# Optimization experiments

Hardware: AMD Instinct MI355X
Metric: run time of the kernel (lower is better)

## Reference

```python
import jax, jax.numpy as jnp
import numpy as np

H = 16          # num_attention_heads
HD = 64         # attention_head_size
ALPHA = 1.5
BANDWIDTH = 1.0
A_EXP = 0.5     # sinkhorn-like exponent 'a'
DIST_SCALE = float(HD)  # alpha < 2 => scale by head_size
EPS = 1e-12     # F.normalize eps


def setup_inputs() -> dict:
    key = jax.random.key(0)
    ks = jax.random.split(key, 5)
    B, L, D = 2, 1024, 1024
    w_scale = 0.02  # keep distances in a non-degenerate range for the power-law kernel
    x = jax.random.normal(ks[0], (B, L, D), dtype=jnp.float32)
    WQ = jax.random.normal(ks[1], (D, D), dtype=jnp.float32) * w_scale
    WK = jax.random.normal(ks[2], (D, D), dtype=jnp.float32) * w_scale
    WV = jax.random.normal(ks[3], (D, D), dtype=jnp.float32) * w_scale
    WO = jax.random.normal(ks[4], (D, D), dtype=jnp.float32) * w_scale
    z = jnp.zeros((D,), dtype=jnp.float32)
    return {"x": x, "WQ": WQ, "bQ": z, "WK": WK, "bK": z,
            "WV": WV, "bV": z, "WO": WO, "bO": z}


def _heads(t, B, L):
    # [B, L, H*HD] -> [B, H, L, HD]
    return t.reshape(B, L, H, HD).transpose(0, 2, 1, 3)


def reference(x, WQ, bQ, WK, bK, WV, bV, WO, bO):
    B, L, D = x.shape
    q = _heads(x @ WQ + bQ, B, L)   # [B,H,L,HD]
    k = _heads(x @ WK + bK, B, L)
    v = _heads(x @ WV + bV, B, L)

    # torch.cdist(q, k, p=2): pairwise euclidean distance [B,H,L,L]
    q2 = jnp.sum(q * q, axis=-1)                      # [B,H,L]
    k2 = jnp.sum(k * k, axis=-1)                      # [B,H,L]
    qk = jnp.einsum('bhid,bhjd->bhij', q, k)          # [B,H,L,L]
    d2 = q2[..., :, None] + k2[..., None, :] - 2.0 * qk
    g_dist = jnp.sqrt(jnp.maximum(d2, EPS)) / DIST_SCALE

    # alpha < 2: power-law kernel (1 + g/sqrt(bw))^(-(d_intrinsic + alpha))
    attn_score = (1.0 + g_dist / np.sqrt(BANDWIDTH)) ** (-(HD + ALPHA))

    # a > 0: Sinkhorn-style row/col renormalization
    N_R = jnp.sum(attn_score, axis=-1)                # [B,H,L] row sums
    N_C = jnp.sum(attn_score, axis=-2)                # [B,H,L] col sums
    K_tilde = (N_R ** (-A_EXP))[..., :, None] * attn_score * (N_C ** (-A_EXP))[..., None, :]

    # F.normalize(p=1, dim=3); entries are positive so |.| sum == sum
    attention_probs = K_tilde / jnp.maximum(jnp.sum(K_tilde, axis=-1, keepdims=True), EPS)

    out = jnp.einsum('bhij,bhjd->bhid', attention_probs, v)   # [B,H,L,HD]
    out = out.transpose(0, 2, 1, 3).reshape(B, L, H * HD)
    return out @ WO + bO
```

## Files before the change

### kernel.cpp

```cpp
#include <hip/hip_runtime.h>
#include <math.h>


typedef __attribute__((ext_vector_type(8))) short short8;
typedef __attribute__((ext_vector_type(4))) float f32x4;

__device__ inline unsigned short f2bf(float f) {
  unsigned int u = __float_as_uint(f);
  unsigned int r = (u + 0x7FFFu + ((u >> 16) & 1u)) >> 16;
  return (unsigned short)r;
}
__device__ inline float bf2f(unsigned short s) {
  return __uint_as_float(((unsigned int)s) << 16);
}
__device__ inline float score_fn(float dot, float sq) {
  float d2 = fmaxf(fmaf(-2.f, dot, sq), 1e-12f);
  float sd = __builtin_amdgcn_sqrtf(d2);
  float lg = __builtin_amdgcn_logf(fmaf(sd, 0.015625f, 1.0f));
  return __builtin_amdgcn_exp2f(-65.5f * lg);
}
__device__ inline unsigned int cvtpk(float lo, float hi) {
  unsigned int r;
  asm("v_cvt_pk_bf16_f32 %0, %1, %2" : "=v"(r) : "v"(lo), "v"(hi));
  return r;
}
#define GLD16(lptr, gptr)                                                      \
  __builtin_amdgcn_global_load_lds(                                            \
      (const __attribute__((address_space(1))) void*)(gptr),                   \
      (__attribute__((address_space(3))) void*)(lptr), 16, 0, 0)

__global__ __launch_bounds__(256) void cvt_f32_bf16(const float* __restrict__ in,
                                                    unsigned short* __restrict__ out) {
  int i = blockIdx.x * 256 + threadIdx.x;
  float4 v = ((const float4*)in)[i];
  out[4 * i + 0] = f2bf(v.x);
  out[4 * i + 1] = f2bf(v.y);
  out[4 * i + 2] = f2bf(v.z);
  out[4 * i + 3] = f2bf(v.w);
}

__global__ __launch_bounds__(256) void wtrans4(const float* __restrict__ W0,
                                               const float* __restrict__ W1,
                                               const float* __restrict__ W2,
                                               const float* __restrict__ W3,
                                               unsigned short* __restrict__ T0,
                                               unsigned short* __restrict__ T1,
                                               unsigned short* __restrict__ T2,
                                               unsigned short* __restrict__ T3) {
  int z = blockIdx.z;
  const float* W = z == 0 ? W0 : z == 1 ? W1 : z == 2 ? W2 : W3;
  unsigned short* WT = z == 0 ? T0 : z == 1 ? T1 : z == 2 ? T2 : T3;
  __shared__ float T[32][33];
  int k0 = blockIdx.x * 32, n0 = blockIdx.y * 32;
  int c = threadIdx.x & 31, r8 = threadIdx.x >> 5;
#pragma unroll
  for (int it = 0; it < 4; ++it) {
    int rr = r8 + it * 8;
    T[rr][c] = W[(size_t)(k0 + rr) * 1024 + n0 + c];
  }
  __syncthreads();
#pragma unroll
  for (int it = 0; it < 4; ++it) {
    int rr = r8 + it * 8;
    WT[(size_t)(n0 + rr) * 1024 + k0 + c] = f2bf(T[c][rr]);
  }
}

__global__ __launch_bounds__(256) void gemm_st(const unsigned short* __restrict__ A,
                                               const unsigned short* __restrict__ B0,
                                               const unsigned short* __restrict__ B1,
                                               const unsigned short* __restrict__ B2,
                                               const float* __restrict__ c0,
                                               const float* __restrict__ c1,
                                               const float* __restrict__ c2,
                                               void* __restrict__ Y0,
                                               void* __restrict__ Y1,
                                               void* __restrict__ Y2,
                                               int m0, int m1, int m2) {
  int z = blockIdx.z;
  const unsigned short* BT = z == 0 ? B0 : z == 1 ? B1 : B2;
  const float* bias = z == 0 ? c0 : z == 1 ? c1 : c2;
  void* Y = z == 0 ? Y0 : z == 1 ? Y1 : Y2;
  int mode = z == 0 ? m0 : z == 1 ? m1 : m2;

  __shared__ __align__(16) unsigned short As[2][64 * 64];
  __shared__ __align__(16) unsigned short Bs[2][64 * 64];
  int tid = threadIdx.x;
  int w = tid >> 6, l = tid & 63, g = l >> 4, l15 = l & 15;
  int bm = blockIdx.x * 64, bn = blockIdx.y * 64;
  const int arow = w * 16 + l15;
  const int x7 = l15 & 7;

  const int i0s = tid, i1s = 256 + tid;
  const int r0 = i0s >> 3, s0 = (i0s & 7) ^ (r0 & 7);
  const int r1 = i1s >> 3, s1 = (i1s & 7) ^ (r1 & 7);

  GLD16(&As[0][i0s * 8], &A[(size_t)(bm + r0) * 1024 + s0 * 8]);
  GLD16(&As[0][i1s * 8], &A[(size_t)(bm + r1) * 1024 + s1 * 8]);
  GLD16(&Bs[0][i0s * 8], &BT[(size_t)(bn + r0) * 1024 + s0 * 8]);
  GLD16(&Bs[0][i1s * 8], &BT[(size_t)(bn + r1) * 1024 + s1 * 8]);

  f32x4 acc[4];
#pragma unroll
  for (int t = 0; t < 4; ++t)
#pragma unroll
    for (int r = 0; r < 4; ++r) acc[t][r] = 0.f;

  __syncthreads();
  for (int t = 0; t < 16; ++t) {
    int cur = t & 1;
    if (t < 15) {
      int kn = (t + 1) * 64;
      GLD16(&As[cur ^ 1][i0s * 8], &A[(size_t)(bm + r0) * 1024 + kn + s0 * 8]);
      GLD16(&As[cur ^ 1][i1s * 8], &A[(size_t)(bm + r1) * 1024 + kn + s1 * 8]);
      GLD16(&Bs[cur ^ 1][i0s * 8], &BT[(size_t)(bn + r0) * 1024 + kn + s0 * 8]);
      GLD16(&Bs[cur ^ 1][i1s * 8], &BT[(size_t)(bn + r1) * 1024 + kn + s1 * 8]);
    }
#pragma unroll
    for (int kc = 0; kc < 2; ++kc) {
      short8 a = *(const short8*)&As[cur][arow * 64 + ((kc * 4 + g) ^ x7) * 8];
#pragma unroll
      for (int tt = 0; tt < 4; ++tt) {
        short8 b = *(const short8*)&Bs[cur][(tt * 16 + l15) * 64 + ((kc * 4 + g) ^ x7) * 8];
        acc[tt] = __builtin_amdgcn_mfma_f32_16x16x32_bf16(a, b, acc[tt], 0, 0, 0);
      }
    }
    __syncthreads();
  }

#pragma unroll
  for (int t = 0; t < 4; ++t) {
    int n = bn + 16 * t + l15;
    float bv = bias[n];
#pragma unroll
    for (int r = 0; r < 4; ++r) {
      int m = bm + w * 16 + 4 * g + r;
      float v = acc[t][r] + bv;
      if (mode == 0) {
        int b = m >> 10, ll = m & 1023, h = n >> 6, hd = n & 63;
        ((unsigned short*)Y)[(((size_t)(b * 16 + h) * 1024) + ll) * 64 + hd] = f2bf(v);
      } else if (mode == 1) {
        int b = m >> 10, ll = m & 1023, h = n >> 6, hd = n & 63;
        int jp = (ll & ~31) | (((ll >> 2) & 3) * 8 + ((ll >> 4) & 1) * 4 + (ll & 3));
        ((unsigned short*)Y)[(((size_t)(b * 16 + h) * 64) + hd) * 1024 + jp] = f2bf(v);
      } else {
        ((float*)Y)[(size_t)m * 1024 + n] = v;
      }
    }
  }
}

__global__ __launch_bounds__(256) void sqnorm(const unsigned short* __restrict__ Qb,
                                              const unsigned short* __restrict__ Kb,
                                              float* __restrict__ q2,
                                              float* __restrict__ k2) {
  int row = blockIdx.x * 256 + threadIdx.x;
  const unsigned short* src = blockIdx.y ? Kb : Qb;
  float* dst = blockIdx.y ? k2 : q2;
  const short8* p = (const short8*)&src[(size_t)row * 64];
  float s = 0.f;
#pragma unroll
  for (int c = 0; c < 8; ++c) {
    short8 v = p[c];
#pragma unroll
    for (int e = 0; e < 8; ++e) {
      float f = bf2f((unsigned short)v[e]);
      s = fmaf(f, f, s);
    }
  }
  dst[row] = s;
}

__global__ __launch_bounds__(256) void colsum_mfma(const unsigned short* __restrict__ Qb,
                                                   const unsigned short* __restrict__ Kb,
                                                   const float* __restrict__ q2,
                                                   const float* __restrict__ k2,
                                                   float* __restrict__ rnc) {
  __shared__ __align__(16) unsigned short Qd[2][64 * 64];
  __shared__ __align__(16) float q2s[1024];
  int bh = blockIdx.x, jt = blockIdx.y;
  int tid = threadIdx.x, w = tid >> 6, l = tid & 63;
  int g = l >> 4, l15 = l & 15;
  const int x7 = l15 & 7;
  const unsigned short* Qp = Qb + (size_t)bh * 65536;
  const unsigned short* Kp = Kb + (size_t)bh * 65536;
  int j = jt * 64 + w * 16 + l15;

  const int i0s = tid, i1s = 256 + tid;
  const int r0 = i0s >> 3, s0 = (i0s & 7) ^ (r0 & 7);
  const int r1 = i1s >> 3, s1 = (i1s & 7) ^ (r1 & 7);

  GLD16(&q2s[tid * 4], q2 + (size_t)bh * 1024 + tid * 4);
  GLD16(&Qd[0][i0s * 8], Qp + (size_t)r0 * 64 + s0 * 8);
  GLD16(&Qd[0][i1s * 8], Qp + (size_t)r1 * 64 + s1 * 8);

  short8 bk0 = *(const short8*)&Kp[(size_t)j * 64 + 8 * g];
  short8 bk1 = *(const short8*)&Kp[(size_t)j * 64 + 32 + 8 * g];
  float k2j = k2[(size_t)bh * 1024 + j];
  float colacc = 0.f;

  __syncthreads();
  for (int t = 0; t < 16; ++t) {
    int cur = t & 1;
    if (t < 15) {
      int inx = (t + 1) * 64;
      GLD16(&Qd[cur ^ 1][i0s * 8], Qp + (size_t)(inx + r0) * 64 + s0 * 8);
      GLD16(&Qd[cur ^ 1][i1s * 8], Qp + (size_t)(inx + r1) * 64 + s1 * 8);
    }
    const unsigned short* Ql = Qd[cur];
#pragma unroll
    for (int tp = 0; tp < 4; ++tp) {
      int rowb = (16 * tp + l15) * 64;
      short8 a0 = *(const short8*)&Ql[rowb + ((g) ^ x7) * 8];
      short8 a1 = *(const short8*)&Ql[rowb + ((4 + g) ^ x7) * 8];
      f32x4 cf;
#pragma unroll
      for (int r = 0; r < 4; ++r) cf[r] = 0.f;
      cf = __builtin_amdgcn_mfma_f32_16x16x32_bf16(a0, bk0, cf, 0, 0, 0);
      cf = __builtin_amdgcn_mfma_f32_16x16x32_bf16(a1, bk1, cf, 0, 0, 0);
      float4 qv = *(const float4*)&q2s[t * 64 + 16 * tp + 4 * g];
      colacc += score_fn(cf[0], qv.x + k2j);
      colacc += score_fn(cf[1], qv.y + k2j);
      colacc += score_fn(cf[2], qv.z + k2j);
      colacc += score_fn(cf[3], qv.w + k2j);
    }
    __syncthreads();
  }
  colacc += __shfl_xor(colacc, 16);
  colacc += __shfl_xor(colacc, 32);
  if (l < 16) rnc[(size_t)bh * 1024 + jt * 64 + w * 16 + l] = __builtin_amdgcn_rsqf(colacc);
}

__global__ __launch_bounds__(256) void attn_mfma(const unsigned short* __restrict__ Qb,
                                                 const unsigned short* __restrict__ Kb,
                                                 const unsigned short* __restrict__ VTp,
                                                 const float* __restrict__ q2,
                                                 const float* __restrict__ k2,
                                                 const float* __restrict__ rnc,
                                                 unsigned short* __restrict__ AO) {
  __shared__ __align__(16) unsigned short Kd[2][64 * 64];
  __shared__ __align__(16) unsigned short Vd[2][64 * 64];
  __shared__ __align__(16) float k2s[1024];
  __shared__ __align__(16) float rns[1024];
  int bh = blockIdx.x;
  int tid = threadIdx.x, w = tid >> 6, l = tid & 63;
  int g = l >> 4, l15 = l & 15;
  const int x7 = l15 & 7;
  int it0 = blockIdx.y * 64 + w * 16;
  const unsigned short* Qp = Qb + (size_t)bh * 65536;
  const unsigned short* Kp = Kb + (size_t)bh * 65536;
  const unsigned short* Vp = VTp + (size_t)bh * 65536;
  int b = bh >> 4, h = bh & 15;

  const int i0s = tid, i1s = 256 + tid;
  const int r0 = i0s >> 3, s0 = (i0s & 7) ^ (r0 & 7);
  const int r1 = i1s >> 3, s1 = (i1s & 7) ^ (r1 & 7);

  GLD16(&k2s[tid * 4], k2 + (size_t)bh * 1024 + tid * 4);
  GLD16(&rns[tid * 4], rnc + (size_t)bh * 1024 + tid * 4);
  GLD16(&Kd[0][i0s * 8], Kp + (size_t)r0 * 64 + s0 * 8);
  GLD16(&Kd[0][i1s * 8], Kp + (size_t)r1 * 64 + s1 * 8);
  GLD16(&Vd[0][i0s * 8], Vp + (size_t)r0 * 1024 + s0 * 8);
  GLD16(&Vd[0][i1s * 8], Vp + (size_t)r1 * 1024 + s1 * 8);

  short8 bq0 = *(const short8*)&Qp[(size_t)(it0 + l15) * 64 + 8 * g];
  short8 bq1 = *(const short8*)&Qp[(size_t)(it0 + l15) * 64 + 32 + 8 * g];
  float q2l = q2[(size_t)bh * 1024 + it0 + l15];

  f32x4 o[4];
#pragma unroll
  for (int t = 0; t < 4; ++t)
#pragma unroll
    for (int r = 0; r < 4; ++r) o[t][r] = 0.f;
  float dacc = 0.f;

  __syncthreads();
  for (int t = 0; t < 16; ++t) {
    int cur = t & 1;
    if (t < 15) {
      int j0n = (t + 1) * 64;
      GLD16(&Kd[cur ^ 1][i0s * 8], Kp + (size_t)(j0n + r0) * 64 + s0 * 8);
      GLD16(&Kd[cur ^ 1][i1s * 8], Kp + (size_t)(j0n + r1) * 64 + s1 * 8);
      GLD16(&Vd[cur ^ 1][i0s * 8], Vp + (size_t)r0 * 1024 + j0n + s0 * 8);
      GLD16(&Vd[cur ^ 1][i1s * 8], Vp + (size_t)r1 * 1024 + j0n + s1 * 8);
    }
    const unsigned short* Kl = Kd[cur];
    const unsigned short* Vl = Vd[cur];
    int j0 = t * 64;
    float sc[16];
#pragma unroll
    for (int tp = 0; tp < 4; ++tp) {
      int rowb = (16 * tp + l15) * 64;
      short8 a0 = *(const short8*)&Kl[rowb + ((g) ^ x7) * 8];
      short8 a1 = *(const short8*)&Kl[rowb + ((4 + g) ^ x7) * 8];
      f32x4 cf;
#pragma unroll
      for (int r = 0; r < 4; ++r) cf[r] = 0.f;
      cf = __builtin_amdgcn_mfma_f32_16x16x32_bf16(a0, bq0, cf, 0, 0, 0);
      cf = __builtin_amdgcn_mfma_f32_16x16x32_bf16(a1, bq1, cf, 0, 0, 0);
      float4 kv = *(const float4*)&k2s[j0 + 16 * tp + 4 * g];
      float4 rv = *(const float4*)&rns[j0 + 16 * tp + 4 * g];
      sc[tp * 4 + 0] = score_fn(cf[0], q2l + kv.x) * rv.x;
      sc[tp * 4 + 1] = score_fn(cf[1], q2l + kv.y) * rv.y;
      sc[tp * 4 + 2] = score_fn(cf[2], q2l + kv.z) * rv.z;
      sc[tp * 4 + 3] = score_fn(cf[3], q2l + kv.w) * rv.w;
    }
#pragma unroll
    for (int i = 0; i < 16; ++i) dacc += sc[i];
    int pi0[4], pi1[4];
    pi0[0] = (int)cvtpk(sc[0], sc[1]);
    pi0[1] = (int)cvtpk(sc[2], sc[3]);
    pi0[2] = (int)cvtpk(sc[4], sc[5]);
    pi0[3] = (int)cvtpk(sc[6], sc[7]);
    pi1[0] = (int)cvtpk(sc[8], sc[9]);
    pi1[1] = (int)cvtpk(sc[10], sc[11]);
    pi1[2] = (int)cvtpk(sc[12], sc[13]);
    pi1[3] = (int)cvtpk(sc[14], sc[15]);
    short8 pa0 = *(short8*)pi0;
    short8 pa1 = *(short8*)pi1;
#pragma unroll
    for (int tt = 0; tt < 4; ++tt) {
      int rowb = (16 * tt + l15) * 64;
      short8 v0 = *(const short8*)&Vl[rowb + ((g) ^ x7) * 8];
      short8 v1 = *(const short8*)&Vl[rowb + ((4 + g) ^ x7) * 8];
      o[tt] = __builtin_amdgcn_mfma_f32_16x16x32_bf16(pa0, v0, o[tt], 0, 0, 0);
      o[tt] = __builtin_amdgcn_mfma_f32_16x16x32_bf16(pa1, v1, o[tt], 0, 0, 0);
    }
    __syncthreads();
  }

  dacc += __shfl_xor(dacc, 16);
  dacc += __shfl_xor(dacc, 32);
  float dv[4];
#pragma unroll
  for (int r = 0; r < 4; ++r) dv[r] = __shfl(dacc, 4 * g + r);

#pragma unroll
  for (int t = 0; t < 4; ++t) {
#pragma unroll
    for (int r = 0; r < 4; ++r) {
      int m = b * 1024 + it0 + 4 * g + r;
      int n = h * 64 + t * 16 + l15;
      AO[(size_t)m * 1024 + n] = f2bf(o[t][r] / dv[r]);
    }
  }
}

extern "C" void kernel_launch(void* const* d_in, const int* in_sizes, int n_in,
                              void* d_out, int out_size, void* d_ws, size_t ws_size,
                              hipStream_t stream) {
  const float* x  = (const float*)d_in[0];
  const float* WQ = (const float*)d_in[1];
  const float* bQ = (const float*)d_in[2];
  const float* WK = (const float*)d_in[3];
  const float* bK = (const float*)d_in[4];
  const float* WV = (const float*)d_in[5];
  const float* bV = (const float*)d_in[6];
  const float* WO = (const float*)d_in[7];
  const float* bO = (const float*)d_in[8];

  char* base = (char*)d_ws;
  unsigned short* xb  = (unsigned short*)(base);
  unsigned short* WQT = (unsigned short*)(base + (4u  << 20));
  unsigned short* WKT = (unsigned short*)(base + (6u  << 20));
  unsigned short* WVT = (unsigned short*)(base + (8u  << 20));
  unsigned short* WOT = (unsigned short*)(base + (10u << 20));
  unsigned short* Qb  = (unsigned short*)(base + (12u << 20));
  unsigned short* Kb  = (unsigned short*)(base + (16u << 20));
  unsigned short* VTp = (unsigned short*)(base + (20u << 20));
  unsigned short* AOb = (unsigned short*)(base + (24u << 20));
  float* q2  = (float*)(base + (28u << 20));
  float* k2  = (float*)(base + (28u << 20) + (128u << 10));
  float* rnc = (float*)(base + (28u << 20) + (256u << 10));

  cvt_f32_bf16<<<2048, 256, 0, stream>>>(x, xb);
  wtrans4<<<dim3(32, 32, 4), 256, 0, stream>>>(WQ, WK, WV, WO, WQT, WKT, WVT, WOT);

  gemm_st<<<dim3(32, 16, 3), 256, 0, stream>>>(xb, WQT, WKT, WVT, bQ, bK, bV,
                                               Qb, Kb, VTp, 0, 0, 1);

  sqnorm<<<dim3(128, 2), 256, 0, stream>>>(Qb, Kb, q2, k2);
  colsum_mfma<<<dim3(32, 16), 256, 0, stream>>>(Qb, Kb, q2, k2, rnc);
  attn_mfma<<<dim3(32, 16), 256, 0, stream>>>(Qb, Kb, VTp, q2, k2, rnc, AOb);

  gemm_st<<<dim3(32, 16, 1), 256, 0, stream>>>(AOb, WOT, WOT, WOT, bO, bO, bO,
                                               d_out, d_out, d_out, 2, 2, 2);
}
```

Measured before the change: 121.6 us.

## Enlarge projection GEMM tiles to 128x128 with 2x2 warp layout

Replaces the 64x64 block tile GEMM with a 128x128 tile, BK=32 and a new XOR swizzle. Each wave now computes a 64x64 sub-tile using 4x4 MFMA accumulators, which raises register reuse of A and B fragments and halves global/LDS traffic per FLOP. The cost is far fewer blocks (384 for QKV, 128 for the output projection) on a device with 256 CUs, which can leave the output GEMM under-occupied, and higher register pressure.

```diff
diff --git a/kernel.cpp b/kernel.cpp
--- a/kernel.cpp
+++ b/kernel.cpp
@@ -66,7 +66,7 @@
   }
 }
 
-__global__ __launch_bounds__(256) void gemm_st(const unsigned short* __restrict__ A,
+__global__ __launch_bounds__(256) void gemm128(const unsigned short* __restrict__ A,
                                                const unsigned short* __restrict__ B0,
                                                const unsigned short* __restrict__ B1,
                                                const unsigned short* __restrict__ B2,
@@ -83,68 +83,77 @@
   void* Y = z == 0 ? Y0 : z == 1 ? Y1 : Y2;
   int mode = z == 0 ? m0 : z == 1 ? m1 : m2;
 
-  __shared__ __align__(16) unsigned short As[2][64 * 64];
-  __shared__ __align__(16) unsigned short Bs[2][64 * 64];
+  __shared__ __align__(16) unsigned short As[2][128 * 32];
+  __shared__ __align__(16) unsigned short Bs[2][128 * 32];
   int tid = threadIdx.x;
   int w = tid >> 6, l = tid & 63, g = l >> 4, l15 = l & 15;
-  int bm = blockIdx.x * 64, bn = blockIdx.y * 64;
-  const int arow = w * 16 + l15;
-  const int x7 = l15 & 7;
-
-  const int i0s = tid, i1s = 256 + tid;
-  const int r0 = i0s >> 3, s0 = (i0s & 7) ^ (r0 & 7);
-  const int r1 = i1s >> 3, s1 = (i1s & 7) ^ (r1 & 7);
-
-  GLD16(&As[0][i0s * 8], &A[(size_t)(bm + r0) * 1024 + s0 * 8]);
-  GLD16(&As[0][i1s * 8], &A[(size_t)(bm + r1) * 1024 + s1 * 8]);
-  GLD16(&Bs[0][i0s * 8], &BT[(size_t)(bn + r0) * 1024 + s0 * 8]);
-  GLD16(&Bs[0][i1s * 8], &BT[(size_t)(bn + r1) * 1024 + s1 * 8]);
-
-  f32x4 acc[4];
-#pragma unroll
-  for (int t = 0; t < 4; ++t)
-#pragma unroll
-    for (int r = 0; r < 4; ++r) acc[t][r] = 0.f;
-
+  int wm = w >> 1, wn = w & 1;
+  int bm = blockIdx.x * 128, bn = blockIdx.y * 128;
+
+  const int i0 = tid, i1 = tid + 256;
+  const int r0 = i0 >> 2, c0s = (i0 & 3) ^ ((r0 ^ (r0 >> 2)) & 3);
+  const int r1 = i1 >> 2, c1s = (i1 & 3) ^ ((r1 ^ (r1 >> 2)) & 3);
+  const int swz = (l15 ^ (l15 >> 2)) & 3;
+
+  GLD16(&As[0][i0 * 8], &A[(size_t)(bm + r0) * 1024 + c0s * 8]);
+  GLD16(&As[0][i1 * 8], &A[(size_t)(bm + r1) * 1024 + c1s * 8]);
+  GLD16(&Bs[0][i0 * 8], &BT[(size_t)(bn + r0) * 1024 + c0s * 8]);
+  GLD16(&Bs[0][i1 * 8], &BT[(size_t)(bn + r1) * 1024 + c1s * 8]);
+
+  f32x4 acc[4][4];
+#pragma unroll
+  for (int mi = 0; mi < 4; ++mi)
+#pragma unroll
+    for (int ni = 0; ni < 4; ++ni)
+#pragma unroll
+      for (int r = 0; r < 4; ++r) acc[mi][ni][r] = 0.f;
+
+  const int cread = ((g ^ swz) & 3) * 8;
   __syncthreads();
-  for (int t = 0; t < 16; ++t) {
+  for (int t = 0; t < 32; ++t) {
     int cur = t & 1;
-    if (t < 15) {
-      int kn = (t + 1) * 64;
-      GLD16(&As[cur ^ 1][i0s * 8], &A[(size_t)(bm + r0) * 1024 + kn + s0 * 8]);
-      GLD16(&As[cur ^ 1][i1s * 8], &A[(size_t)(bm + r1) * 1024 + kn + s1 * 8]);
-      GLD16(&Bs[cur ^ 1][i0s * 8], &BT[(size_t)(bn + r0) * 1024 + kn + s0 * 8]);
-      GLD16(&Bs[cur ^ 1][i1s * 8], &BT[(size_t)(bn + r1) * 1024 + kn + s1 * 8]);
-    }
-#pragma unroll
-    for (int kc = 0; kc < 2; ++kc) {
-      short8 a = *(const short8*)&As[cur][arow * 64 + ((kc * 4 + g) ^ x7) * 8];
-#pragma unroll
-      for (int tt = 0; tt < 4; ++tt) {
-        short8 b = *(const short8*)&Bs[cur][(tt * 16 + l15) * 64 + ((kc * 4 + g) ^ x7) * 8];
-        acc[tt] = __builtin_amdgcn_mfma_f32_16x16x32_bf16(a, b, acc[tt], 0, 0, 0);
-      }
-    }
+    if (t < 31) {
+      int kn = (t + 1) * 32;
+      GLD16(&As[cur ^ 1][i0 * 8], &A[(size_t)(bm + r0) * 1024 + kn + c0s * 8]);
+      GLD16(&As[cur ^ 1][i1 * 8], &A[(size_t)(bm + r1) * 1024 + kn + c1s * 8]);
+      GLD16(&Bs[cur ^ 1][i0 * 8], &BT[(size_t)(bn + r0) * 1024 + kn + c0s * 8]);
+      GLD16(&Bs[cur ^ 1][i1 * 8], &BT[(size_t)(bn + r1) * 1024 + kn + c1s * 8]);
+    }
+    short8 a[4], b[4];
+#pragma unroll
+    for (int mi = 0; mi < 4; ++mi)
+      a[mi] = *(const short8*)&As[cur][(wm * 64 + mi * 16 + l15) * 32 + cread];
+#pragma unroll
+    for (int ni = 0; ni < 4; ++ni)
+      b[ni] = *(const short8*)&Bs[cur][(wn * 64 + ni * 16 + l15) * 32 + cread];
+#pragma unroll
+    for (int mi = 0; mi < 4; ++mi)
+#pragma unroll
+      for (int ni = 0; ni < 4; ++ni)
+        acc[mi][ni] = __builtin_amdgcn_mfma_f32_16x16x32_bf16(a[mi], b[ni], acc[mi][ni], 0, 0, 0);
     __syncthreads();
   }
 
 #pragma unroll
-  for (int t = 0; t < 4; ++t) {
-    int n = bn + 16 * t + l15;
+  for (int ni = 0; ni < 4; ++ni) {
+    int n = bn + wn * 64 + ni * 16 + l15;
     float bv = bias[n];
 #pragma unroll
-    for (int r = 0; r < 4; ++r) {
-      int m = bm + w * 16 + 4 * g + r;
-      float v = acc[t][r] + bv;
-      if (mode == 0) {
-        int b = m >> 10, ll = m & 1023, h = n >> 6, hd = n & 63;
-        ((unsigned short*)Y)[(((size_t)(b * 16 + h) * 1024) + ll) * 64 + hd] = f2bf(v);
-      } else if (mode == 1) {
-        int b = m >> 10, ll = m & 1023, h = n >> 6, hd = n & 63;
-        int jp = (ll & ~31) | (((ll >> 2) & 3) * 8 + ((ll >> 4) & 1) * 4 + (ll & 3));
-        ((unsigned short*)Y)[(((size_t)(b * 16 + h) * 64) + hd) * 1024 + jp] = f2bf(v);
-      } else {
-        ((float*)Y)[(size_t)m * 1024 + n] = v;
+    for (int mi = 0; mi < 4; ++mi) {
+#pragma unroll
+      for (int r = 0; r < 4; ++r) {
+        int m = bm + wm * 64 + mi * 16 + 4 * g + r;
+        float v = acc[mi][ni][r] + bv;
+        if (mode == 0) {
+          int b = m >> 10, ll = m & 1023, h = n >> 6, hd = n & 63;
+          ((unsigned short*)Y)[(((size_t)(b * 16 + h) * 1024) + ll) * 64 + hd] = f2bf(v);
+        } else if (mode == 1) {
+          int b = m >> 10, ll = m & 1023, h = n >> 6, hd = n & 63;
+          int jp = (ll & ~31) | (((ll >> 2) & 3) * 8 + ((ll >> 4) & 1) * 4 + (ll & 3));
+          ((unsigned short*)Y)[(((size_t)(b * 16 + h) * 64) + hd) * 1024 + jp] = f2bf(v);
+        } else {
+          ((float*)Y)[(size_t)m * 1024 + n] = v;
+        }
       }
     }
   }
@@ -376,13 +385,13 @@
   cvt_f32_bf16<<<2048, 256, 0, stream>>>(x, xb);
   wtrans4<<<dim3(32, 32, 4), 256, 0, stream>>>(WQ, WK, WV, WO, WQT, WKT, WVT, WOT);
 
-  gemm_st<<<dim3(32, 16, 3), 256, 0, stream>>>(xb, WQT, WKT, WVT, bQ, bK, bV,
-                                               Qb, Kb, VTp, 0, 0, 1);
+  gemm128<<<dim3(16, 8, 3), 256, 0, stream>>>(xb, WQT, WKT, WVT, bQ, bK, bV,
+                                              Qb, Kb, VTp, 0, 0, 1);
 
   sqnorm<<<dim3(128, 2), 256, 0, stream>>>(Qb, Kb, q2, k2);
   colsum_mfma<<<dim3(32, 16), 256, 0, stream>>>(Qb, Kb, q2, k2, rnc);
   attn_mfma<<<dim3(32, 16), 256, 0, stream>>>(Qb, Kb, VTp, q2, k2, rnc, AOb);
 
-  gemm_st<<<dim3(32, 16, 1), 256, 0, stream>>>(AOb, WOT, WOT, WOT, bO, bO, bO,
-                                               d_out, d_out, d_out, 2, 2, 2);
-}
+  gemm128<<<dim3(16, 8, 1), 256, 0, stream>>>(AOb, WOT, WOT, WOT, bO, bO, bO,
+                                              d_out, d_out, d_out, 2, 2, 2);
+}
```

After: 126.9 us. +4.3%, slower.

## Use 128x128 K64 double-buffered GEMM for QKV projection

Applied to the files above, without the earlier changes.

Adds a new GEMM kernel with 128x128 output tiles, K-step 64, 512 threads, double-buffered LDS with XOR swizzle and async global-to-LDS loads, and uses it for the fused QKV projection in place of the smaller-tile gemm_st. Larger tiles raise operand reuse per LDS load and cut global traffic. The trade-off is fewer blocks (384) and higher LDS and register use per block, which may lower occupancy.

```diff
diff --git a/kernel.cpp b/kernel.cpp
--- a/kernel.cpp
+++ b/kernel.cpp
@@ -63,6 +63,102 @@
   for (int it = 0; it < 4; ++it) {
     int rr = r8 + it * 8;
     WT[(size_t)(n0 + rr) * 1024 + k0 + c] = f2bf(T[c][rr]);
+  }
+}
+
+__global__ __launch_bounds__(512, 2) void gemm128k64(const unsigned short* __restrict__ A,
+                                                     const unsigned short* __restrict__ B0,
+                                                     const unsigned short* __restrict__ B1,
+                                                     const unsigned short* __restrict__ B2,
+                                                     const float* __restrict__ c0,
+                                                     const float* __restrict__ c1,
+                                                     const float* __restrict__ c2,
+                                                     void* __restrict__ Y0,
+                                                     void* __restrict__ Y1,
+                                                     void* __restrict__ Y2,
+                                                     int m0, int m1, int m2) {
+  int z = blockIdx.z;
+  const unsigned short* BT = z == 0 ? B0 : z == 1 ? B1 : B2;
+  const float* bias = z == 0 ? c0 : z == 1 ? c1 : c2;
+  void* Y = z == 0 ? Y0 : z == 1 ? Y1 : Y2;
+  int mode = z == 0 ? m0 : z == 1 ? m1 : m2;
+
+  __shared__ __align__(16) unsigned short As[2][128 * 64];
+  __shared__ __align__(16) unsigned short Bs[2][128 * 64];
+  int tid = threadIdx.x;
+  int w = tid >> 6, l = tid & 63, g = l >> 4, l15 = l & 15;
+  int wm = w >> 2, wn = w & 3;
+  int bm = blockIdx.x * 128, bn = blockIdx.y * 128;
+  const int x7 = l15 & 7;
+
+  const int i0 = tid, i1 = tid + 512;
+  const int r0 = i0 >> 3, s0 = (i0 & 7) ^ (r0 & 7);
+  const int r1 = i1 >> 3, s1 = (i1 & 7) ^ (r1 & 7);
+
+  GLD16(&As[0][i0 * 8], &A[(size_t)(bm + r0) * 1024 + s0 * 8]);
+  GLD16(&As[0][i1 * 8], &A[(size_t)(bm + r1) * 1024 + s1 * 8]);
+  GLD16(&Bs[0][i0 * 8], &BT[(size_t)(bn + r0) * 1024 + s0 * 8]);
+  GLD16(&Bs[0][i1 * 8], &BT[(size_t)(bn + r1) * 1024 + s1 * 8]);
+
+  f32x4 acc[4][2];
+#pragma unroll
+  for (int mi = 0; mi < 4; ++mi)
+#pragma unroll
+    for (int ni = 0; ni < 2; ++ni)
+#pragma unroll
+      for (int r = 0; r < 4; ++r) acc[mi][ni][r] = 0.f;
+
+  __syncthreads();
+  for (int t = 0; t < 16; ++t) {
+    int cur = t & 1;
+    if (t < 15) {
+      int kn = (t + 1) * 64;
+      GLD16(&As[cur ^ 1][i0 * 8], &A[(size_t)(bm + r0) * 1024 + kn + s0 * 8]);
+      GLD16(&As[cur ^ 1][i1 * 8], &A[(size_t)(bm + r1) * 1024 + kn + s1 * 8]);
+      GLD16(&Bs[cur ^ 1][i0 * 8], &BT[(size_t)(bn + r0) * 1024 + kn + s0 * 8]);
+      GLD16(&Bs[cur ^ 1][i1 * 8], &BT[(size_t)(bn + r1) * 1024 + kn + s1 * 8]);
+    }
+#pragma unroll
+    for (int kc = 0; kc < 2; ++kc) {
+      const int cread = (((kc << 2) + g) ^ x7) * 8;
+      short8 a[4], b[2];
+#pragma unroll
+      for (int mi = 0; mi < 4; ++mi)
+        a[mi] = *(const short8*)&As[cur][(wm * 64 + mi * 16 + l15) * 64 + cread];
+#pragma unroll
+      for (int ni = 0; ni < 2; ++ni)
+        b[ni] = *(const short8*)&Bs[cur][(wn * 32 + ni * 16 + l15) * 64 + cread];
+#pragma unroll
+      for (int mi = 0; mi < 4; ++mi)
+#pragma unroll
+        for (int ni = 0; ni < 2; ++ni)
+          acc[mi][ni] = __builtin_amdgcn_mfma_f32_16x16x32_bf16(a[mi], b[ni], acc[mi][ni], 0, 0, 0);
+    }
+    __syncthreads();
+  }
+
+#pragma unroll
+  for (int ni = 0; ni < 2; ++ni) {
+    int n = bn + wn * 32 + ni * 16 + l15;
+    float bv = bias[n];
+#pragma unroll
+    for (int mi = 0; mi < 4; ++mi) {
+#pragma unroll
+      for (int r = 0; r < 4; ++r) {
+        int m = bm + wm * 64 + mi * 16 + 4 * g + r;
+        float v = acc[mi][ni][r] + bv;
+        if (mode == 0) {
+          int b = m >> 10, ll = m & 1023, h = n >> 6, hd = n & 63;
+          ((unsigned short*)Y)[(((size_t)(b * 16 + h) * 1024) + ll) * 64 + hd] = f2bf(v);
+        } else if (mode == 1) {
+          int b = m >> 10, ll = m & 1023, h = n >> 6, hd = n & 63;
+          int jp = (ll & ~31) | (((ll >> 2) & 3) * 8 + ((ll >> 4) & 1) * 4 + (ll & 3));
+          ((unsigned short*)Y)[(((size_t)(b * 16 + h) * 64) + hd) * 1024 + jp] = f2bf(v);
+        } else {
+          ((float*)Y)[(size_t)m * 1024 + n] = v;
+        }
+      }
+    }
   }
 }
 
@@ -376,8 +472,8 @@
   cvt_f32_bf16<<<2048, 256, 0, stream>>>(x, xb);
   wtrans4<<<dim3(32, 32, 4), 256, 0, stream>>>(WQ, WK, WV, WO, WQT, WKT, WVT, WOT);
 
-  gemm_st<<<dim3(32, 16, 3), 256, 0, stream>>>(xb, WQT, WKT, WVT, bQ, bK, bV,
-                                               Qb, Kb, VTp, 0, 0, 1);
+  gemm128k64<<<dim3(16, 8, 3), 512, 0, stream>>>(xb, WQT, WKT, WVT, bQ, bK, bV,
+                                                 Qb, Kb, VTp, 0, 0, 1);
 
   sqnorm<<<dim3(128, 2), 256, 0, stream>>>(Qb, Kb, q2, k2);
   colsum_mfma<<<dim3(32, 16), 256, 0, stream>>>(Qb, Kb, q2, k2, rnc);
```

New measurement: 109.6 us. 1.11x faster.
